# Performance work log

Hardware: AMD Instinct MI355X
Metric: run time of the kernel (lower is better)

## Reference

```python
import jax, jax.numpy as jnp
import numpy as np

NL, D, H, DK, L, F, P, NC, PS = 2, 128, 8, 16, 197, 256, 8, 1000, 16
EPS = 1e-5


def _ln(x, w, b):
    m = jnp.mean(x, -1, keepdims=True)
    v = jnp.mean((x - m) ** 2, -1, keepdims=True)
    return (x - m) * jax.lax.rsqrt(v + EPS) * w + b


def _trop_lin(x, W, b):
    # max-plus (tropical) linear: y_o = max_i (x_i + W[o, i]) + b_o
    return jnp.max(x[..., None, :] + W, axis=-1) + b


def _forward(x, patch_w, patch_b, cls_token, pos_embed, bn_gamma, bn_beta, bn_run_max, bn_run_range,
             n1_w, n1_b, n2_w, n2_b, wq, bq, wk, bk, wv, bv, wo, bo, gate_w, gate_b, temp,
             tu_w, tu_b, lf_a, lf_c, lf_gate, cu_w, cu_b, fg_w, fg_b, dn_w, dn_b,
             fn_w, fn_b, head_w, head_b):
    B, C, Hh, Ww = x.shape
    p = PS
    # patchify: [B,C,H,W] -> [B,num_patches,C*p*p]
    xp = x.reshape(B, C, Hh // p, p, Ww // p, p).transpose(0, 2, 4, 1, 3, 5).reshape(B, -1, C * p * p)
    h = xp @ patch_w.T + patch_b
    h = jnp.concatenate([jnp.broadcast_to(cls_token, (B, 1, D)), h], axis=1) + pos_embed
    # TropicalBatchNorm (eval mode, running buffers)
    h = bn_gamma * ((h - bn_run_max) / (bn_run_range + EPS)) + bn_beta
    scale = DK ** -0.5
    for i in range(NL):
        hn = _ln(h, n1_w[i], n1_b[i])
        Q = _trop_lin(hn, wq[i], bq[i]).reshape(B, L, H, DK).transpose(0, 2, 1, 3)
        K = _trop_lin(hn, wk[i], bk[i]).reshape(B, L, H, DK).transpose(0, 2, 1, 3)
        V = (hn @ wv[i].T + bv[i]).reshape(B, L, H, DK).transpose(0, 2, 1, 3)
        cs = jnp.einsum('bhqd,bhkd->bhqk', Q, K) * scale
        # tropical max-plus scores: max_d(Q_q + K_k)  -> [B,H,L,L]
        ts = jnp.max(Q[:, :, :, None, :] + K[:, :, None, :, :], axis=-1) * scale
        g = jax.nn.sigmoid(hn @ gate_w[i].T + gate_b[i]).transpose(0, 2, 1)[..., None]  # [B,H,L,1]
        attn = jax.nn.softmax((g * ts + (1.0 - g) * cs) / temp[i][None, :, None, None], axis=-1)
        out = jnp.einsum('bhqk,bhkd->bhqd', attn, V).transpose(0, 2, 1, 3).reshape(B, L, D)
        h = h + (out @ wo[i].T + bo[i])
        hn2 = _ln(h, n2_w[i], n2_b[i])
        z = _trop_lin(hn2, tu_w[i], tu_b[i])                 # [B,L,F]
        zp = z[:, :, None, :] * lf_a[i] + lf_c[i]            # [B,L,P,F]
        gl = jax.nn.sigmoid(lf_gate[i])
        trop = gl * jnp.max(zp, axis=2) + (1.0 - gl) * jnp.min(zp, axis=2)
        classical = jax.nn.gelu(hn2 @ cu_w[i].T + cu_b[i], approximate=False)
        gf = jax.nn.sigmoid(hn2 @ fg_w[i].T + fg_b[i])
        fused = gf * trop + (1.0 - gf) * classical
        h = h + (fused @ dn_w[i].T + dn_b[i])
    h = _ln(h, fn_w, fn_b)
    return h[:, 0] @ head_w.T + head_b


def setup_inputs() -> dict:
    ks = iter(jax.random.split(jax.random.key(0), 64))
    rn = lambda shape, s=0.02: jax.random.normal(next(ks), shape, jnp.float32) * s
    return dict(
        x=jax.random.normal(next(ks), (4, 3, 224, 224), jnp.float32),
        patch_w=rn((D, 3 * PS * PS)), patch_b=jnp.zeros((D,), jnp.float32),
        cls_token=rn((1, 1, D)), pos_embed=rn((1, L, D)),
        bn_gamma=jnp.ones((D,), jnp.float32), bn_beta=jnp.zeros((D,), jnp.float32),
        bn_run_max=jnp.zeros((D,), jnp.float32), bn_run_range=jnp.ones((D,), jnp.float32),
        n1_w=jnp.ones((NL, D), jnp.float32) + rn((NL, D)), n1_b=rn((NL, D)),
        n2_w=jnp.ones((NL, D), jnp.float32) + rn((NL, D)), n2_b=rn((NL, D)),
        wq=rn((NL, D, D)), bq=rn((NL, D)),
        wk=rn((NL, D, D)), bk=rn((NL, D)),
        wv=rn((NL, D, D)), bv=rn((NL, D)),
        wo=rn((NL, D, D)), bo=rn((NL, D)),
        gate_w=rn((NL, H, D)), gate_b=2.0 + rn((NL, H)),
        temp=1.0 + 0.1 * jax.random.uniform(next(ks), (NL, H), jnp.float32),
        tu_w=rn((NL, F, D)), tu_b=rn((NL, F)),
        lf_a=rn((NL, P, F), 0.5), lf_c=rn((NL, P, F), 0.1), lf_gate=rn((NL, F), 0.5),
        cu_w=rn((NL, F, D)), cu_b=rn((NL, F)),
        fg_w=rn((NL, F, D)), fg_b=2.0 + rn((NL, F)),
        dn_w=rn((NL, D, F)), dn_b=rn((NL, D)),
        fn_w=jnp.ones((D,), jnp.float32) + rn((D,)), fn_b=rn((D,)),
        head_w=rn((NC, D)), head_b=jnp.zeros((NC,), jnp.float32),
    )


def reference(x, patch_w, patch_b, cls_token, pos_embed, bn_gamma, bn_beta, bn_run_max, bn_run_range,
              n1_w, n1_b, n2_w, n2_b, wq, bq, wk, bk, wv, bv, wo, bo, gate_w, gate_b, temp,
              tu_w, tu_b, lf_a, lf_c, lf_gate, cu_w, cu_b, fg_w, fg_b, dn_w, dn_b,
              fn_w, fn_b, head_w, head_b):
    return _forward(x, patch_w, patch_b, cls_token, pos_embed, bn_gamma, bn_beta, bn_run_max, bn_run_range,
                    n1_w, n1_b, n2_w, n2_b, wq, bq, wk, bk, wv, bv, wo, bo, gate_w, gate_b, temp,
                    tu_w, tu_b, lf_a, lf_c, lf_gate, cu_w, cu_b, fg_w, fg_b, dn_w, dn_b,
                    fn_w, fn_b, head_w, head_b)
```

## Files before the change

### kernel.cpp

```cpp
#include <hip/hip_runtime.h>
#include <math.h>

#define EPSF 1e-5f

__device__ __forceinline__ float sigm(float v){ return 1.f/(1.f+__expf(-v)); }

#define WS_H    0
#define WS_Q    100864
#define WS_K    201728
#define WS_V    302592
#define WS_G    403456
#define WS_AO   409760
#define WS_PWT  510624
#define WS_WQT  608928
#define WS_WKT  641696
#define WS_WVT  674464
#define WS_WOT  707232
#define WS_GWT  740000
#define WS_TUT  742048
#define WS_CUT  807584
#define WS_FGT  873120
#define WS_DNT  938656
#define WS_HDT  1004192

__global__ __launch_bounds__(256) void k_tr(
    const float* __restrict__ pw, const float* __restrict__ wq, const float* __restrict__ wk,
    const float* __restrict__ wv, const float* __restrict__ wo, const float* __restrict__ gw,
    const float* __restrict__ tu, const float* __restrict__ cu, const float* __restrict__ fg,
    const float* __restrict__ dn, const float* __restrict__ hd, float* __restrict__ ws)
{
    __shared__ float tile[32][33];
    int tn = blockIdx.x, t = threadIdx.x;

    if (tn >= 608) {
        for (int i=t;i<2048;i+=256){
            int m=i>>10, rem=i&1023, k=rem>>3, hh=rem&7;
            ws[WS_GWT + m*1024 + k*8 + hh] = gw[m*1024 + hh*128 + k];
        }
        return;
    }

    const float* srcp; long dstoff; int N, K, NR, nt, kt;
    if (tn < 96) {
        srcp=pw; dstoff=WS_PWT; N=128; K=768; NR=128; nt=tn/24; kt=tn%24;
    } else if (tn < 224) {
        int i2=tn-96, inst=i2>>4, lt=i2&15, m2=inst>>1;
        srcp = (m2==0)?wq:(m2==1)?wk:(m2==2)?wv:wo;
        srcp += (inst&1)*16384;
        dstoff = WS_WQT + (long)m2*32768 + (inst&1)*16384;
        N=128; K=128; NR=128; nt=lt>>2; kt=lt&3;
    } else if (tn < 416) {
        int i2=tn-224, inst=i2>>5, lt=i2&31, m2=inst>>1;
        srcp = (m2==0)?tu:(m2==1)?cu:fg;
        srcp += (inst&1)*32768;
        dstoff = WS_TUT + (long)m2*65536 + (inst&1)*32768;
        N=256; K=128; NR=256; nt=lt>>2; kt=lt&3;
    } else if (tn < 480) {
        int i2=tn-416, inst=i2>>5, lt=i2&31;
        srcp = dn + inst*32768; dstoff = WS_DNT + (long)inst*32768;
        N=128; K=256; NR=128; nt=lt>>3; kt=lt&7;
    } else {
        int lt=tn-480; srcp=hd; dstoff=WS_HDT; N=1000; K=128; NR=1000; nt=lt>>2; kt=lt&3;
    }

    int n0=nt*32, k0=kt*32;
    int tr=t>>3, tc=(t&7)*4;
    float4 v={0.f,0.f,0.f,0.f};
    if (n0+tr < NR) v = *(const float4*)(srcp + (size_t)(n0+tr)*K + k0 + tc);
    tile[tr][tc]=v.x; tile[tr][tc+1]=v.y; tile[tr][tc+2]=v.z; tile[tr][tc+3]=v.w;
    __syncthreads();
    int kr=t>>3, nc=(t&7)*4;
    float o0=tile[nc][kr], o1=tile[nc+1][kr], o2=tile[nc+2][kr], o3=tile[nc+3][kr];
    float* dp = ws + dstoff + (size_t)(k0+kr)*N + n0 + nc;
    if (n0+nc+3 < NR) {
        float4 o4={o0,o1,o2,o3};
        *(float4*)dp = o4;
    } else {
        if (n0+nc   < NR) dp[0]=o0;
        if (n0+nc+1 < NR) dp[1]=o1;
        if (n0+nc+2 < NR) dp[2]=o2;
        if (n0+nc+3 < NR) dp[3]=o3;
    }
}

__device__ __forceinline__ void ln_rows(const float hv[4],
    const float* __restrict__ lw, const float* __restrict__ lb,
    float* hnS, float* red, int t)
{
    int d = t & 127;
    if (t < 128) {
        float s[4], s2[4];
        #pragma unroll
        for (int r=0;r<4;++r){ s[r]=hv[r]; s2[r]=hv[r]*hv[r]; }
        #pragma unroll
        for (int o=1;o<64;o<<=1){
            #pragma unroll
            for (int r=0;r<4;++r){ s[r]+=__shfl_xor(s[r],o); s2[r]+=__shfl_xor(s2[r],o); }
        }
        if ((t & 63)==0){
            int wid = t>>6;
            #pragma unroll
            for (int r=0;r<4;++r){ red[r*2+wid]=s[r]; red[8+r*2+wid]=s2[r]; }
        }
    }
    __syncthreads();
    if (t < 128) {
        #pragma unroll
        for (int r=0;r<4;++r){
            float S=red[r*2]+red[r*2+1], S2=red[8+r*2]+red[8+r*2+1];
            float mu=S*(1.f/128.f), var=S2*(1.f/128.f)-mu*mu;
            float rr=rsqrtf(var+EPSF);
            hnS[r*128+d]=(hv[r]-mu)*rr*lw[d]+lb[d];
        }
    }
    __syncthreads();
}

__device__ __forceinline__ void qkvT512(const float* hnS, float* pacc, int r0, int t,
    const float* __restrict__ wqT, const float* __restrict__ bq,
    const float* __restrict__ wkT, const float* __restrict__ bk,
    const float* __restrict__ wvT, const float* __restrict__ bv,
    const float* __restrict__ gwT, const float* __restrict__ gb,
    float* __restrict__ Q, float* __restrict__ Kg, float* __restrict__ V,
    float* __restrict__ g)
{
    if (t < 384) {
        int mat = t >> 7, q4i = t & 31, ks = (t >> 5) & 3;
        const float* wT = (mat==0) ? wqT : (mat==1) ? wkT : wvT;
        const float4* w4 = (const float4*)wT + q4i;
        float4 acc[4];
        if (mat < 2) {
            #pragma unroll
            for (int r=0;r<4;++r){ acc[r].x=acc[r].y=acc[r].z=acc[r].w=-1e30f; }
            #pragma unroll
            for (int kb=0;kb<4;++kb){
                float4 wv8[8];
                #pragma unroll
                for (int j=0;j<8;++j) wv8[j]=w4[(ks*32+kb*8+j)*32];
                #pragma unroll
                for (int j=0;j<8;++j){
                    float4 w=wv8[j];
                    #pragma unroll
                    for (int r=0;r<4;++r){
                        float av = hnS[r*128 + ks*32+kb*8+j];
                        acc[r].x=fmaxf(acc[r].x,av+w.x); acc[r].y=fmaxf(acc[r].y,av+w.y);
                        acc[r].z=fmaxf(acc[r].z,av+w.z); acc[r].w=fmaxf(acc[r].w,av+w.w);
                    }
                }
            }
        } else {
            #pragma unroll
            for (int r=0;r<4;++r){ acc[r].x=acc[r].y=acc[r].z=acc[r].w=0.f; }
            #pragma unroll
            for (int kb=0;kb<4;++kb){
                float4 wv8[8];
                #pragma unroll
                for (int j=0;j<8;++j) wv8[j]=w4[(ks*32+kb*8+j)*32];
                #pragma unroll
                for (int j=0;j<8;++j){
                    float4 w=wv8[j];
                    #pragma unroll
                    for (int r=0;r<4;++r){
                        float av = hnS[r*128 + ks*32+kb*8+j];
                        acc[r].x=fmaf(av,w.x,acc[r].x); acc[r].y=fmaf(av,w.y,acc[r].y);
                        acc[r].z=fmaf(av,w.z,acc[r].z); acc[r].w=fmaf(av,w.w,acc[r].w);
                    }
                }
            }
        }
        #pragma unroll
        for (int r=0;r<4;++r)
            *(float4*)(pacc + mat*2048 + ks*512 + r*128 + q4i*4) = acc[r];
    } else {
        int u = t & 127, r = u>>5, hh=(u>>2)&7, ks=u&3;
        const float* a = hnS + r*128;
        float acc = 0.f;
        #pragma unroll
        for (int kb=0;kb<4;++kb){
            float wv8[8];
            #pragma unroll
            for (int j=0;j<8;++j) wv8[j]=gwT[(ks*32+kb*8+j)*8+hh];
            #pragma unroll
            for (int j=0;j<8;++j) acc = fmaf(a[ks*32+kb*8+j], wv8[j], acc);
        }
        acc += __shfl_xor(acc,1);
        acc += __shfl_xor(acc,2);
        if (ks==0) g[(r0+r)*8+hh] = sigm(acc + gb[hh]);
    }
    __syncthreads();
    if (t < 384) {
        int mat=t>>7, d=t&127;
        float* dst = (mat==0) ? Q : (mat==1) ? Kg : V;
        const float* bias = (mat==0) ? bq : (mat==1) ? bk : bv;
        #pragma unroll
        for (int r=0;r<4;++r){
            float p0 = pacc[mat*2048 + 0*512 + r*128 + d];
            float p1 = pacc[mat*2048 + 1*512 + r*128 + d];
            float p2 = pacc[mat*2048 + 2*512 + r*128 + d];
            float p3 = pacc[mat*2048 + 3*512 + r*128 + d];
            float s = (mat < 2) ? fmaxf(fmaxf(p0,p1), fmaxf(p2,p3))
                                : (p0 + p1 + p2 + p3);
            dst[(size_t)(r0+r)*128 + d] = s + bias[d];
        }
    }
}

__global__ __launch_bounds__(512) void k_p1(
    const float* __restrict__ x, const float* __restrict__ pwT, const float* __restrict__ pb,
    const float* __restrict__ clsT, const float* __restrict__ pos,
    const float* __restrict__ bng, const float* __restrict__ bnb,
    const float* __restrict__ bnm, const float* __restrict__ bnr,
    const float* __restrict__ n1w, const float* __restrict__ n1b,
    const float* __restrict__ wqT, const float* __restrict__ bq,
    const float* __restrict__ wkT, const float* __restrict__ bk,
    const float* __restrict__ wvT, const float* __restrict__ bv,
    const float* __restrict__ gwT, const float* __restrict__ gb,
    float* __restrict__ h, float* __restrict__ Q, float* __restrict__ Kg,
    float* __restrict__ V, float* __restrict__ g)
{
    __shared__ __align__(16) float xp[4*768];
    __shared__ __align__(16) float pacc[8192];
    __shared__ __align__(16) float hnS[512];
    __shared__ float red[16];
    int t = threadIdx.x, r0 = blockIdx.x * 4;

    #pragma unroll
    for (int r=0;r<4;++r){
        int row=r0+r, b=row/197, l=row-b*197;
        if (l>0){
            int patch=l-1, ph=patch/14, pc=patch-ph*14;
            const float* xb = x + (size_t)b*150528 + ph*3584 + pc*16;
            for (int i=t;i<768;i+=512){
                int c=i>>8, rr=(i>>4)&15, cc=i&15;
                xp[r*768+i] = xb[c*50176 + rr*224 + cc];
            }
        }
    }
    __syncthreads();

    {
        int q4i = t & 31, ks = t >> 5;
        float4 acc[4];
        #pragma unroll
        for (int r=0;r<4;++r){ acc[r].x=acc[r].y=acc[r].z=acc[r].w=0.f; }
        const float4* w4 = (const float4*)pwT + q4i;
        #pragma unroll
        for (int kb=0;kb<6;++kb){
            float4 wv8[8];
            #pragma unroll
            for (int j=0;j<8;++j) wv8[j]=w4[(ks*48+kb*8+j)*32];
            #pragma unroll
            for (int j=0;j<8;++j){
                float4 w=wv8[j];
                #pragma unroll
                for (int r=0;r<4;++r){
                    float av = xp[r*768 + ks*48+kb*8+j];
                    acc[r].x=fmaf(av,w.x,acc[r].x); acc[r].y=fmaf(av,w.y,acc[r].y);
                    acc[r].z=fmaf(av,w.z,acc[r].z); acc[r].w=fmaf(av,w.w,acc[r].w);
                }
            }
        }
        #pragma unroll
        for (int r=0;r<4;++r)
            *(float4*)(pacc + (ks*4+r)*128 + q4i*4) = acc[r];
    }
    __syncthreads();

    float hres[4]={0.f,0.f,0.f,0.f};
    if (t < 128){
        int d=t;
        #pragma unroll
        for (int r=0;r<4;++r){
            int row=r0+r, l=row%197;
            float s = 0.f;
            #pragma unroll
            for (int ks=0;ks<16;++ks) s += pacc[(ks*4+r)*128+d];
            float v = (l==0) ? clsT[d] : (s + pb[d]);
            v += pos[l*128+d];
            v = bng[d]*((v-bnm[d])/(bnr[d]+EPSF))+bnb[d];
            hres[r]=v;
            h[row*128+d]=v;
        }
    }
    ln_rows(hres, n1w, n1b, hnS, red, t);
    qkvT512(hnS, pacc, r0, t, wqT,bq,wkT,bk,wvT,bv,gwT,gb, Q,Kg,V,g);
}

__global__ __launch_bounds__(256) void k_attn(
    const float* __restrict__ Qd, const float* __restrict__ Kd,
    const float* __restrict__ Vd, const float* __restrict__ gd,
    const float* __restrict__ tempL, float* __restrict__ ao)
{
    __shared__ __align__(16) float Ks[197*20];
    __shared__ __align__(16) float Vs[197*20];
    int bid = blockIdx.x, t = threadIdx.x;
    int qc = bid % 7, bh = bid / 7, hh = bh & 7, b = bh >> 3;
    size_t base = (size_t)(b*197)*128 + hh*16;

    {
        const float4* ksrc=(const float4*)(Kd+base);
        const float4* vsrc=(const float4*)(Vd+base);
        float4* kdst=(float4*)Ks; float4* vdst=(float4*)Vs;
        for (int idx=t; idx<788; idx+=256){
            int l=idx>>2, jj=idx&3;
            kdst[l*5+jj]=ksrc[l*32+jj];
            vdst[l*5+jj]=vsrc[l*32+jj];
        }
    }
    __syncthreads();

    int q = qc*32 + (t>>3), j8 = t&7;
    if (q >= 197) return;

    float Qr[16];
    {
        const float4* qp=(const float4*)(Qd+base+(size_t)q*128);
        #pragma unroll
        for (int u=0;u<4;++u){
            float4 v=qp[u];
            Qr[4*u]=v.x; Qr[4*u+1]=v.y; Qr[4*u+2]=v.z; Qr[4*u+3]=v.w;
        }
    }
    float gq = gd[(b*197+q)*8+hh];
    float it = 0.25f / tempL[hh];
    float gg = gq*it, cg = (1.f-gq)*it;

    float m=-1e30f, lsum=0.f, o[16];
    #pragma unroll
    for (int j=0;j<16;++j) o[j]=0.f;

    for (int k=j8;k<197;k+=8){
        const float4* kr4=(const float4*)(Ks+k*20);
        float4 kv0=kr4[0], kv1=kr4[1], kv2=kr4[2], kv3=kr4[3];
        float kr[16] = {kv0.x,kv0.y,kv0.z,kv0.w, kv1.x,kv1.y,kv1.z,kv1.w,
                        kv2.x,kv2.y,kv2.z,kv2.w, kv3.x,kv3.y,kv3.z,kv3.w};
        float cs=0.f, ts=-1e30f;
        #pragma unroll
        for (int j=0;j<16;++j){
            cs=fmaf(Qr[j],kr[j],cs);
            ts=fmaxf(ts,Qr[j]+kr[j]);
        }
        float sc=fmaf(gg,ts,cg*cs);
        if (sc>m){
            float c=__expf(m-sc);
            lsum*=c;
            #pragma unroll
            for (int j=0;j<16;++j) o[j]*=c;
            m=sc;
        }
        float p=__expf(sc-m);
        lsum+=p;
        const float4* vr4=(const float4*)(Vs+k*20);
        float4 vv0=vr4[0], vv1=vr4[1], vv2=vr4[2], vv3=vr4[3];
        float vr[16] = {vv0.x,vv0.y,vv0.z,vv0.w, vv1.x,vv1.y,vv1.z,vv1.w,
                        vv2.x,vv2.y,vv2.z,vv2.w, vv3.x,vv3.y,vv3.z,vv3.w};
        #pragma unroll
        for (int j=0;j<16;++j) o[j]=fmaf(p,vr[j],o[j]);
    }

    #pragma unroll
    for (int mask=1;mask<8;mask<<=1){
        float mo=__shfl_xor(m,mask), lo=__shfl_xor(lsum,mask);
        float mn=fmaxf(m,mo);
        float ea=__expf(m-mn), eb=__expf(mo-mn);
        lsum=lsum*ea+lo*eb;
        #pragma unroll
        for (int j=0;j<16;++j){
            float oo=__shfl_xor(o[j],mask);
            o[j]=o[j]*ea+oo*eb;
        }
        m=mn;
    }

    if (j8==0){
        float inv=1.f/lsum;
        float* orow=ao+base+(size_t)q*128;
        #pragma unroll
        for (int j=0;j<16;++j) orow[j]=o[j]*inv;
    }
}

template <int FINAL>
__global__ __launch_bounds__(512) void k_p34(
    const float* __restrict__ ao, float* __restrict__ h,
    const float* __restrict__ woT, const float* __restrict__ bo,
    const float* __restrict__ n2w, const float* __restrict__ n2b,
    const float* __restrict__ tuT, const float* __restrict__ tub,
    const float* __restrict__ laA, const float* __restrict__ laC,
    const float* __restrict__ lgG,
    const float* __restrict__ cuT, const float* __restrict__ cub,
    const float* __restrict__ fgT, const float* __restrict__ fgb,
    const float* __restrict__ dnT, const float* __restrict__ dnb,
    const float* __restrict__ nlw, const float* __restrict__ nlb,
    const float* __restrict__ wqT, const float* __restrict__ bq,
    const float* __restrict__ wkT, const float* __restrict__ bk,
    const float* __restrict__ wvT, const float* __restrict__ bv,
    const float* __restrict__ gwT, const float* __restrict__ gb,
    float* __restrict__ Q, float* __restrict__ Kg, float* __restrict__ V,
    float* __restrict__ g,
    const float* __restrict__ hdT, const float* __restrict__ hdb,
    float* __restrict__ out)
{
    __shared__ __align__(16) float aoS[512];
    __shared__ __align__(16) float pacc[8192];
    __shared__ __align__(16) float hnS[512];
    __shared__ __align__(16) float zP[6144];
    __shared__ __align__(16) float fusedS[1024];
    __shared__ float red[16];
    int t = threadIdx.x, r0 = blockIdx.x * 4;

    aoS[t] = ao[(size_t)r0*128 + t];
    __syncthreads();

    {
        int q4i=t&31, ks=t>>5;
        float4 acc[4];
        #pragma unroll
        for (int r=0;r<4;++r){ acc[r].x=acc[r].y=acc[r].z=acc[r].w=0.f; }
        const float4* w4=(const float4*)woT + q4i;
        float4 wv8[8];
        #pragma unroll
        for (int j=0;j<8;++j) wv8[j]=w4[(ks*8+j)*32];
        #pragma unroll
        for (int j=0;j<8;++j){
            float4 w=wv8[j];
            #pragma unroll
            for (int r=0;r<4;++r){
                float av=aoS[r*128 + ks*8+j];
                acc[r].x=fmaf(av,w.x,acc[r].x); acc[r].y=fmaf(av,w.y,acc[r].y);
                acc[r].z=fmaf(av,w.z,acc[r].z); acc[r].w=fmaf(av,w.w,acc[r].w);
            }
        }
        #pragma unroll
        for (int r=0;r<4;++r)
            *(float4*)(pacc + (ks*4+r)*128 + q4i*4) = acc[r];
    }
    __syncthreads();

    float hres[4]={0.f,0.f,0.f,0.f};
    if (t<128){
        int d=t;
        #pragma unroll
        for (int r=0;r<4;++r){
            float s=0.f;
            #pragma unroll
            for (int ks=0;ks<16;++ks) s += pacc[(ks*4+r)*128+d];
            hres[r]=h[(r0+r)*128+d]+s+bo[d];
        }
    }
    ln_rows(hres, n2w, n2b, hnS, red, t);

    {
        int gidx=t>>6, fq=t&63;
        if (gidx < 6) {
            int mat=gidx>>1, ks2=gidx&1;
            const float* wT = (mat==0)? tuT : (mat==1)? cuT : fgT;
            const float4* w4=(const float4*)wT + fq;
            float4 acc[4];
            if (mat==0){
                #pragma unroll
                for (int r=0;r<4;++r){ acc[r].x=acc[r].y=acc[r].z=acc[r].w=-1e30f; }
                #pragma unroll
                for (int kb=0;kb<8;++kb){
                    float4 wv8[8];
                    #pragma unroll
                    for (int j=0;j<8;++j) wv8[j]=w4[(ks2*64+kb*8+j)*64];
                    #pragma unroll
                    for (int j=0;j<8;++j){
                        float4 w=wv8[j];
                        #pragma unroll
                        for (int r=0;r<4;++r){
                            float av=hnS[r*128 + ks2*64+kb*8+j];
                            acc[r].x=fmaxf(acc[r].x,av+w.x); acc[r].y=fmaxf(acc[r].y,av+w.y);
                            acc[r].z=fmaxf(acc[r].z,av+w.z); acc[r].w=fmaxf(acc[r].w,av+w.w);
                        }
                    }
                }
            } else {
                #pragma unroll
                for (int r=0;r<4;++r){ acc[r].x=acc[r].y=acc[r].z=acc[r].w=0.f; }
                #pragma unroll
                for (int kb=0;kb<8;++kb){
                    float4 wv8[8];
                    #pragma unroll
                    for (int j=0;j<8;++j) wv8[j]=w4[(ks2*64+kb*8+j)*64];
                    #pragma unroll
                    for (int j=0;j<8;++j){
                        float4 w=wv8[j];
                        #pragma unroll
                        for (int r=0;r<4;++r){
                            float av=hnS[r*128 + ks2*64+kb*8+j];
                            acc[r].x=fmaf(av,w.x,acc[r].x); acc[r].y=fmaf(av,w.y,acc[r].y);
                            acc[r].z=fmaf(av,w.z,acc[r].z); acc[r].w=fmaf(av,w.w,acc[r].w);
                        }
                    }
                }
            }
            #pragma unroll
            for (int r=0;r<4;++r)
                *(float4*)(zP + mat*2048 + ks2*1024 + r*256 + fq*4) = acc[r];
        }
    }
    __syncthreads();

    #pragma unroll
    for (int s2=0;s2<2;++s2){
        int slot = t + s2*512;
        int r = slot>>8, f = slot&255;
        float z  = fmaxf(zP[r*256+f],        zP[1024+r*256+f]) + tub[f];
        float xc = zP[2048+r*256+f] + zP[3072+r*256+f] + cub[f];
        float gv = zP[4096+r*256+f] + zP[5120+r*256+f] + fgb[f];
        float gl = sigm(lgG[f]);
        float mx=-1e30f, mn=1e30f;
        #pragma unroll
        for (int p=0;p<8;++p){
            float zp=fmaf(z, laA[p*256+f], laC[p*256+f]);
            mx=fmaxf(mx,zp); mn=fminf(mn,zp);
        }
        float trop=gl*mx+(1.f-gl)*mn;
        float cla=0.5f*xc*(1.f+erff(xc*0.70710678118654752f));
        float gf=sigm(gv);
        fusedS[r*256+f]=gf*trop+(1.f-gf)*cla;
    }
    __syncthreads();

    {
        int q4i=t&31, ks=t>>5;
        float4 acc[4];
        #pragma unroll
        for (int r=0;r<4;++r){ acc[r].x=acc[r].y=acc[r].z=acc[r].w=0.f; }
        const float4* w4=(const float4*)dnT + q4i;
        #pragma unroll
        for (int kb=0;kb<2;++kb){
            float4 wv8[8];
            #pragma unroll
            for (int j=0;j<8;++j) wv8[j]=w4[(ks*16+kb*8+j)*32];
            #pragma unroll
            for (int j=0;j<8;++j){
                float4 w=wv8[j];
                #pragma unroll
                for (int r=0;r<4;++r){
                    float av=fusedS[r*256 + ks*16+kb*8+j];
                    acc[r].x=fmaf(av,w.x,acc[r].x); acc[r].y=fmaf(av,w.y,acc[r].y);
                    acc[r].z=fmaf(av,w.z,acc[r].z); acc[r].w=fmaf(av,w.w,acc[r].w);
                }
            }
        }
        __syncthreads();
        #pragma unroll
        for (int r=0;r<4;++r)
            *(float4*)(pacc + (ks*4+r)*128 + q4i*4) = acc[r];
    }
    __syncthreads();
    if (t<128){
        int d=t;
        #pragma unroll
        for (int r=0;r<4;++r){
            float s=0.f;
            #pragma unroll
            for (int ks=0;ks<16;++ks) s += pacc[(ks*4+r)*128+d];
            hres[r]+=s+dnb[d];
            if (!FINAL) h[(r0+r)*128+d]=hres[r];
        }
    }
    ln_rows(hres, nlw, nlb, hnS, red, t);

    if (!FINAL) {
        qkvT512(hnS, pacc, r0, t, wqT,bq,wkT,bk,wvT,bv,gwT,gb, Q,Kg,V,g);
    } else {
        int crow=-1, cb2=0;
        #pragma unroll
        for (int r=0;r<4;++r){
            int row=r0+r;
            if (row==0 || row==197 || row==394 || row==591){ crow=r; cb2=row/197; }
        }
        if (crow>=0 && t<500){
            const float2* w2=(const float2*)hdT + t;
            const float* a = hnS + crow*128;
            float acc0=hdb[2*t], acc1=hdb[2*t+1];
            #pragma unroll
            for (int kb=0;kb<16;++kb){
                float2 wv8[8];
                #pragma unroll
                for (int j=0;j<8;++j) wv8[j]=w2[(kb*8+j)*500];
                #pragma unroll
                for (int j=0;j<8;++j){
                    float av=a[kb*8+j];
                    acc0=fmaf(av,wv8[j].x,acc0); acc1=fmaf(av,wv8[j].y,acc1);
                }
            }
            out[cb2*1000+2*t]=acc0;
            out[cb2*1000+2*t+1]=acc1;
        }
    }
}

extern "C" void kernel_launch(void* const* d_in, const int* in_sizes, int n_in,
                              void* d_out, int out_size, void* d_ws, size_t ws_size,
                              hipStream_t stream)
{
    const float* x        = (const float*)d_in[0];
    const float* patch_w  = (const float*)d_in[1];
    const float* patch_b  = (const float*)d_in[2];
    const float* cls_tok  = (const float*)d_in[3];
    const float* pos_emb  = (const float*)d_in[4];
    const float* bn_gamma = (const float*)d_in[5];
    const float* bn_beta  = (const float*)d_in[6];
    const float* bn_rmax  = (const float*)d_in[7];
    const float* bn_rrng  = (const float*)d_in[8];
    const float* n1_w     = (const float*)d_in[9];
    const float* n1_b     = (const float*)d_in[10];
    const float* n2_w     = (const float*)d_in[11];
    const float* n2_b     = (const float*)d_in[12];
    const float* wq       = (const float*)d_in[13];
    const float* bq       = (const float*)d_in[14];
    const float* wk       = (const float*)d_in[15];
    const float* bk       = (const float*)d_in[16];
    const float* wv       = (const float*)d_in[17];
    const float* bv       = (const float*)d_in[18];
    const float* wo       = (const float*)d_in[19];
    const float* bo       = (const float*)d_in[20];
    const float* gate_w   = (const float*)d_in[21];
    const float* gate_b   = (const float*)d_in[22];
    const float* temp     = (const float*)d_in[23];
    const float* tu_w     = (const float*)d_in[24];
    const float* tu_b     = (const float*)d_in[25];
    const float* lf_a     = (const float*)d_in[26];
    const float* lf_c     = (const float*)d_in[27];
    const float* lf_gate  = (const float*)d_in[28];
    const float* cu_w     = (const float*)d_in[29];
    const float* cu_b     = (const float*)d_in[30];
    const float* fg_w     = (const float*)d_in[31];
    const float* fg_b     = (const float*)d_in[32];
    const float* dn_w     = (const float*)d_in[33];
    const float* dn_b     = (const float*)d_in[34];
    const float* fn_w     = (const float*)d_in[35];
    const float* fn_b     = (const float*)d_in[36];
    const float* head_w   = (const float*)d_in[37];
    const float* head_b   = (const float*)d_in[38];

    float* ws = (float*)d_ws;
    float* h   = ws + WS_H;
    float* Q   = ws + WS_Q;
    float* Kb  = ws + WS_K;
    float* V   = ws + WS_V;
    float* g   = ws + WS_G;
    float* ao  = ws + WS_AO;
    float* out = (float*)d_out;

    k_tr<<<609, 256, 0, stream>>>(patch_w, wq, wk, wv, wo, gate_w,
                                  tu_w, cu_w, fg_w, dn_w, head_w, ws);

    k_p1<<<197, 512, 0, stream>>>(x, ws+WS_PWT, patch_b, cls_tok, pos_emb,
                                  bn_gamma, bn_beta, bn_rmax, bn_rrng,
                                  n1_w, n1_b,
                                  ws+WS_WQT, bq, ws+WS_WKT, bk, ws+WS_WVT, bv,
                                  ws+WS_GWT, gate_b,
                                  h, Q, Kb, V, g);

    k_attn<<<224, 256, 0, stream>>>(Q, Kb, V, g, temp, ao);

    k_p34<0><<<197, 512, 0, stream>>>(ao, h,
        ws+WS_WOT, bo, n2_w, n2_b,
        ws+WS_TUT, tu_b, lf_a, lf_c, lf_gate,
        ws+WS_CUT, cu_b, ws+WS_FGT, fg_b, ws+WS_DNT, dn_b,
        n1_w + 128, n1_b + 128,
        ws+WS_WQT+16384, bq + 128, ws+WS_WKT+16384, bk + 128,
        ws+WS_WVT+16384, bv + 128, ws+WS_GWT+1024, gate_b + 8,
        Q, Kb, V, g, nullptr, nullptr, nullptr);

    k_attn<<<224, 256, 0, stream>>>(Q, Kb, V, g, temp + 8, ao);

    k_p34<1><<<197, 512, 0, stream>>>(ao, h,
        ws+WS_WOT+16384, bo + 128, n2_w + 128, n2_b + 128,
        ws+WS_TUT+32768, tu_b + 256, lf_a + 2048, lf_c + 2048, lf_gate + 256,
        ws+WS_CUT+32768, cu_b + 256, ws+WS_FGT+32768, fg_b + 256,
        ws+WS_DNT+32768, dn_b + 128,
        fn_w, fn_b,
        nullptr, nullptr, nullptr, nullptr, nullptr, nullptr, nullptr, nullptr,
        Q, Kb, V, g, ws+WS_HDT, head_b, out);
}
```

Before: 79.33 us.

## Process eight token rows per block in row-wise kernels to improve weight reuse

The patch-embed/QKV kernel and the attention-output/FFN kernels now handle 8 rows per block instead of 4, halving the grid to 99 blocks. Each weight load from global memory is reused across twice as many rows, and all 512 threads now take part in the reductions and LayerNorm instead of only 128. Shared buffers are merged into one union array and boundary guards are added for the padded last block. In exchange, each thread holds more accumulator registers and the smaller grid leaves more compute units idle.

```diff
diff --git a/kernel.cpp b/kernel.cpp
--- a/kernel.cpp
+++ b/kernel.cpp
@@ -83,40 +83,33 @@
     }
 }
 
-__device__ __forceinline__ void ln_rows(const float hv[4],
+__device__ __forceinline__ void ln8(const float hv[2],
     const float* __restrict__ lw, const float* __restrict__ lb,
-    float* hnS, float* red, int t)
+    float* hnS, float* redS, float* redS2, int t)
 {
-    int d = t & 127;
-    if (t < 128) {
-        float s[4], s2[4];
-        #pragma unroll
-        for (int r=0;r<4;++r){ s[r]=hv[r]; s2[r]=hv[r]*hv[r]; }
-        #pragma unroll
-        for (int o=1;o<64;o<<=1){
-            #pragma unroll
-            for (int r=0;r<4;++r){ s[r]+=__shfl_xor(s[r],o); s2[r]+=__shfl_xor(s2[r],o); }
-        }
-        if ((t & 63)==0){
-            int wid = t>>6;
-            #pragma unroll
-            for (int r=0;r<4;++r){ red[r*2+wid]=s[r]; red[8+r*2+wid]=s2[r]; }
-        }
-    }
-    __syncthreads();
-    if (t < 128) {
-        #pragma unroll
-        for (int r=0;r<4;++r){
-            float S=red[r*2]+red[r*2+1], S2=red[8+r*2]+red[8+r*2+1];
-            float mu=S*(1.f/128.f), var=S2*(1.f/128.f)-mu*mu;
-            float rr=rsqrtf(var+EPSF);
-            hnS[r*128+d]=(hv[r]-mu)*rr*lw[d]+lb[d];
-        }
+    #pragma unroll
+    for (int s=0;s<2;++s){
+        float sm=hv[s], sq=hv[s]*hv[s];
+        #pragma unroll
+        for (int o=1;o<64;o<<=1){ sm+=__shfl_xor(sm,o); sq+=__shfl_xor(sq,o); }
+        if ((t&63)==0){
+            int slot=t+s*512, r=slot>>7, half=(t>>6)&1;
+            redS[r*2+half]=sm; redS2[r*2+half]=sq;
+        }
+    }
+    __syncthreads();
+    #pragma unroll
+    for (int s=0;s<2;++s){
+        int slot=t+s*512, r=slot>>7, d=slot&127;
+        float S=redS[r*2]+redS[r*2+1], S2=redS2[r*2]+redS2[r*2+1];
+        float mu=S*(1.f/128.f), var=S2*(1.f/128.f)-mu*mu;
+        float rr=rsqrtf(var+EPSF);
+        hnS[r*128+d]=(hv[s]-mu)*rr*lw[d]+lb[d];
     }
     __syncthreads();
 }
 
-__device__ __forceinline__ void qkvT512(const float* hnS, float* pacc, int r0, int t,
+__device__ __forceinline__ void qkvT8(const float* hnS, float* uni, int r0, int t,
     const float* __restrict__ wqT, const float* __restrict__ bq,
     const float* __restrict__ wkT, const float* __restrict__ bk,
     const float* __restrict__ wvT, const float* __restrict__ bv,
@@ -128,10 +121,10 @@
         int mat = t >> 7, q4i = t & 31, ks = (t >> 5) & 3;
         const float* wT = (mat==0) ? wqT : (mat==1) ? wkT : wvT;
         const float4* w4 = (const float4*)wT + q4i;
-        float4 acc[4];
+        float4 acc[8];
         if (mat < 2) {
             #pragma unroll
-            for (int r=0;r<4;++r){ acc[r].x=acc[r].y=acc[r].z=acc[r].w=-1e30f; }
+            for (int r=0;r<8;++r){ acc[r].x=acc[r].y=acc[r].z=acc[r].w=-1e30f; }
             #pragma unroll
             for (int kb=0;kb<4;++kb){
                 float4 wv8[8];
@@ -141,7 +134,7 @@
                 for (int j=0;j<8;++j){
                     float4 w=wv8[j];
                     #pragma unroll
-                    for (int r=0;r<4;++r){
+                    for (int r=0;r<8;++r){
                         float av = hnS[r*128 + ks*32+kb*8+j];
                         acc[r].x=fmaxf(acc[r].x,av+w.x); acc[r].y=fmaxf(acc[r].y,av+w.y);
                         acc[r].z=fmaxf(acc[r].z,av+w.z); acc[r].w=fmaxf(acc[r].w,av+w.w);
@@ -150,7 +143,7 @@
             }
         } else {
             #pragma unroll
-            for (int r=0;r<4;++r){ acc[r].x=acc[r].y=acc[r].z=acc[r].w=0.f; }
+            for (int r=0;r<8;++r){ acc[r].x=acc[r].y=acc[r].z=acc[r].w=0.f; }
             #pragma unroll
             for (int kb=0;kb<4;++kb){
                 float4 wv8[8];
@@ -160,7 +153,7 @@
                 for (int j=0;j<8;++j){
                     float4 w=wv8[j];
                     #pragma unroll
-                    for (int r=0;r<4;++r){
+                    for (int r=0;r<8;++r){
                         float av = hnS[r*128 + ks*32+kb*8+j];
                         acc[r].x=fmaf(av,w.x,acc[r].x); acc[r].y=fmaf(av,w.y,acc[r].y);
                         acc[r].z=fmaf(av,w.z,acc[r].z); acc[r].w=fmaf(av,w.w,acc[r].w);
@@ -169,23 +162,23 @@
             }
         }
         #pragma unroll
-        for (int r=0;r<4;++r)
-            *(float4*)(pacc + mat*2048 + ks*512 + r*128 + q4i*4) = acc[r];
+        for (int r=0;r<8;++r)
+            *(float4*)(uni + mat*4096 + ks*1024 + r*128 + q4i*4) = acc[r];
     } else {
-        int u = t & 127, r = u>>5, hh=(u>>2)&7, ks=u&3;
-        const float* a = hnS + r*128;
+        int u = t & 127, r8 = u>>4, hh=(u>>1)&7, ks2=u&1;
+        const float* a = hnS + r8*128;
         float acc = 0.f;
         #pragma unroll
-        for (int kb=0;kb<4;++kb){
+        for (int kb=0;kb<8;++kb){
             float wv8[8];
             #pragma unroll
-            for (int j=0;j<8;++j) wv8[j]=gwT[(ks*32+kb*8+j)*8+hh];
-            #pragma unroll
-            for (int j=0;j<8;++j) acc = fmaf(a[ks*32+kb*8+j], wv8[j], acc);
+            for (int j=0;j<8;++j) wv8[j]=gwT[(ks2*64+kb*8+j)*8+hh];
+            #pragma unroll
+            for (int j=0;j<8;++j) acc = fmaf(a[ks2*64+kb*8+j], wv8[j], acc);
         }
         acc += __shfl_xor(acc,1);
-        acc += __shfl_xor(acc,2);
-        if (ks==0) g[(r0+r)*8+hh] = sigm(acc + gb[hh]);
+        int row=r0+r8;
+        if (ks2==0 && row<788) g[row*8+hh] = sigm(acc + gb[hh]);
     }
     __syncthreads();
     if (t < 384) {
@@ -193,14 +186,15 @@
         float* dst = (mat==0) ? Q : (mat==1) ? Kg : V;
         const float* bias = (mat==0) ? bq : (mat==1) ? bk : bv;
         #pragma unroll
-        for (int r=0;r<4;++r){
-            float p0 = pacc[mat*2048 + 0*512 + r*128 + d];
-            float p1 = pacc[mat*2048 + 1*512 + r*128 + d];
-            float p2 = pacc[mat*2048 + 2*512 + r*128 + d];
-            float p3 = pacc[mat*2048 + 3*512 + r*128 + d];
+        for (int r=0;r<8;++r){
+            float p0 = uni[mat*4096 + 0*1024 + r*128 + d];
+            float p1 = uni[mat*4096 + 1*1024 + r*128 + d];
+            float p2 = uni[mat*4096 + 2*1024 + r*128 + d];
+            float p3 = uni[mat*4096 + 3*1024 + r*128 + d];
             float s = (mat < 2) ? fmaxf(fmaxf(p0,p1), fmaxf(p2,p3))
                                 : (p0 + p1 + p2 + p3);
-            dst[(size_t)(r0+r)*128 + d] = s + bias[d];
+            int row=r0+r;
+            if (row<788) dst[(size_t)row*128 + d] = s + bias[d];
         }
     }
 }
@@ -218,21 +212,24 @@
     float* __restrict__ h, float* __restrict__ Q, float* __restrict__ Kg,
     float* __restrict__ V, float* __restrict__ g)
 {
-    __shared__ __align__(16) float xp[4*768];
-    __shared__ __align__(16) float pacc[8192];
-    __shared__ __align__(16) float hnS[512];
-    __shared__ float red[16];
-    int t = threadIdx.x, r0 = blockIdx.x * 4;
-
-    #pragma unroll
-    for (int r=0;r<4;++r){
-        int row=r0+r, b=row/197, l=row-b*197;
-        if (l>0){
-            int patch=l-1, ph=patch/14, pc=patch-ph*14;
-            const float* xb = x + (size_t)b*150528 + ph*3584 + pc*16;
-            for (int i=t;i<768;i+=512){
-                int c=i>>8, rr=(i>>4)&15, cc=i&15;
-                xp[r*768+i] = xb[c*50176 + rr*224 + cc];
+    __shared__ __align__(16) float xp[8*768];
+    __shared__ __align__(16) float uni[16384];
+    __shared__ __align__(16) float hnS[1024];
+    __shared__ float redS[16], redS2[16];
+    int t = threadIdx.x, r0 = blockIdx.x * 8;
+
+    #pragma unroll
+    for (int r=0;r<8;++r){
+        int row=r0+r;
+        if (row < 788){
+            int b=row/197, l=row-b*197;
+            if (l>0){
+                int patch=l-1, ph=patch/14, pc=patch-ph*14;
+                const float* xb = x + (size_t)b*150528 + ph*3584 + pc*16;
+                for (int i=t;i<768;i+=512){
+                    int c=i>>8, rr=(i>>4)&15, cc=i&15;
+                    xp[r*768+i] = xb[c*50176 + rr*224 + cc];
+                }
             }
         }
     }
@@ -240,9 +237,9 @@
 
     {
         int q4i = t & 31, ks = t >> 5;
-        float4 acc[4];
-        #pragma unroll
-        for (int r=0;r<4;++r){ acc[r].x=acc[r].y=acc[r].z=acc[r].w=0.f; }
+        float4 acc[8];
+        #pragma unroll
+        for (int r=0;r<8;++r){ acc[r].x=acc[r].y=acc[r].z=acc[r].w=0.f; }
         const float4* w4 = (const float4*)pwT + q4i;
         #pragma unroll
         for (int kb=0;kb<6;++kb){
@@ -253,7 +250,7 @@
             for (int j=0;j<8;++j){
                 float4 w=wv8[j];
                 #pragma unroll
-                for (int r=0;r<4;++r){
+                for (int r=0;r<8;++r){
                     float av = xp[r*768 + ks*48+kb*8+j];
                     acc[r].x=fmaf(av,w.x,acc[r].x); acc[r].y=fmaf(av,w.y,acc[r].y);
                     acc[r].z=fmaf(av,w.z,acc[r].z); acc[r].w=fmaf(av,w.w,acc[r].w);
@@ -261,29 +258,28 @@
             }
         }
         #pragma unroll
-        for (int r=0;r<4;++r)
-            *(float4*)(pacc + (ks*4+r)*128 + q4i*4) = acc[r];
-    }
-    __syncthreads();
-
-    float hres[4]={0.f,0.f,0.f,0.f};
-    if (t < 128){
-        int d=t;
-        #pragma unroll
-        for (int r=0;r<4;++r){
-            int row=r0+r, l=row%197;
-            float s = 0.f;
-            #pragma unroll
-            for (int ks=0;ks<16;++ks) s += pacc[(ks*4+r)*128+d];
-            float v = (l==0) ? clsT[d] : (s + pb[d]);
-            v += pos[l*128+d];
-            v = bng[d]*((v-bnm[d])/(bnr[d]+EPSF))+bnb[d];
-            hres[r]=v;
-            h[row*128+d]=v;
-        }
-    }
-    ln_rows(hres, n1w, n1b, hnS, red, t);
-    qkvT512(hnS, pacc, r0, t, wqT,bq,wkT,bk,wvT,bv,gwT,gb, Q,Kg,V,g);
+        for (int r=0;r<8;++r)
+            *(float4*)(uni + (ks*8+r)*128 + q4i*4) = acc[r];
+    }
+    __syncthreads();
+
+    float hres[2];
+    #pragma unroll
+    for (int s=0;s<2;++s){
+        int slot=t+s*512, r=slot>>7, d=slot&127;
+        int row=r0+r, l=row%197;
+        float sm = 0.f;
+        #pragma unroll
+        for (int ks=0;ks<16;++ks) sm += uni[(ks*8+r)*128+d];
+        float v = (l==0) ? clsT[d] : (sm + pb[d]);
+        v += pos[l*128+d];
+        v = bng[d]*((v-bnm[d])/(bnr[d]+EPSF))+bnb[d];
+        hres[s]=v;
+        if (row<788) h[(size_t)row*128+d]=v;
+    }
+    __syncthreads();
+    ln8(hres, n1w, n1b, hnS, redS, redS2, t);
+    qkvT8(hnS, uni, r0, t, wqT,bq,wkT,bk,wvT,bv,gwT,gb, Q,Kg,V,g);
 }
 
 __global__ __launch_bounds__(256) void k_attn(
@@ -401,22 +397,22 @@
     const float* __restrict__ hdT, const float* __restrict__ hdb,
     float* __restrict__ out)
 {
-    __shared__ __align__(16) float aoS[512];
-    __shared__ __align__(16) float pacc[8192];
-    __shared__ __align__(16) float hnS[512];
-    __shared__ __align__(16) float zP[6144];
-    __shared__ __align__(16) float fusedS[1024];
-    __shared__ float red[16];
-    int t = threadIdx.x, r0 = blockIdx.x * 4;
-
-    aoS[t] = ao[(size_t)r0*128 + t];
+    __shared__ __align__(16) float aoS[1024];
+    __shared__ __align__(16) float uni[16384];
+    __shared__ __align__(16) float hnS[1024];
+    __shared__ __align__(16) float fusedS[2048];
+    __shared__ float redS[16], redS2[16];
+    int t = threadIdx.x, r0 = blockIdx.x * 8;
+
+    aoS[t]     = ao[(size_t)r0*128 + t];
+    aoS[t+512] = ao[(size_t)r0*128 + t + 512];
     __syncthreads();
 
     {
         int q4i=t&31, ks=t>>5;
-        float4 acc[4];
-        #pragma unroll
-        for (int r=0;r<4;++r){ acc[r].x=acc[r].y=acc[r].z=acc[r].w=0.f; }
+        float4 acc[8];
+        #pragma unroll
+        for (int r=0;r<8;++r){ acc[r].x=acc[r].y=acc[r].z=acc[r].w=0.f; }
         const float4* w4=(const float4*)woT + q4i;
         float4 wv8[8];
         #pragma unroll
@@ -425,30 +421,29 @@
         for (int j=0;j<8;++j){
             float4 w=wv8[j];
             #pragma unroll
-            for (int r=0;r<4;++r){
+            for (int r=0;r<8;++r){
                 float av=aoS[r*128 + ks*8+j];
                 acc[r].x=fmaf(av,w.x,acc[r].x); acc[r].y=fmaf(av,w.y,acc[r].y);
                 acc[r].z=fmaf(av,w.z,acc[r].z); acc[r].w=fmaf(av,w.w,acc[r].w);
             }
         }
         #pragma unroll
-        for (int r=0;r<4;++r)
-            *(float4*)(pacc + (ks*4+r)*128 + q4i*4) = acc[r];
-    }
-    __syncthreads();
-
-    float hres[4]={0.f,0.f,0.f,0.f};
-    if (t<128){
-        int d=t;
-        #pragma unroll
-        for (int r=0;r<4;++r){
-            float s=0.f;
-            #pragma unroll
-            for (int ks=0;ks<16;++ks) s += pacc[(ks*4+r)*128+d];
-            hres[r]=h[(r0+r)*128+d]+s+bo[d];
-        }
-    }
-    ln_rows(hres, n2w, n2b, hnS, red, t);
+        for (int r=0;r<8;++r)
+            *(float4*)(uni + (ks*8+r)*128 + q4i*4) = acc[r];
+    }
+    __syncthreads();
+
+    float hres[2];
+    #pragma unroll
+    for (int s=0;s<2;++s){
+        int slot=t+s*512, r=slot>>7, d=slot&127;
+        float sm=0.f;
+        #pragma unroll
+        for (int ks=0;ks<16;++ks) sm += uni[(ks*8+r)*128+d];
+        hres[s] = h[(size_t)(r0+r)*128+d] + sm + bo[d];
+    }
+    __syncthreads();
+    ln8(hres, n2w, n2b, hnS, redS, redS2, t);
 
     {
         int gidx=t>>6, fq=t&63;
@@ -456,10 +451,10 @@
             int mat=gidx>>1, ks2=gidx&1;
             const float* wT = (mat==0)? tuT : (mat==1)? cuT : fgT;
             const float4* w4=(const float4*)wT + fq;
-            float4 acc[4];
+            float4 acc[8];
             if (mat==0){
                 #pragma unroll
-                for (int r=0;r<4;++r){ acc[r].x=acc[r].y=acc[r].z=acc[r].w=-1e30f; }
+                for (int r=0;r<8;++r){ acc[r].x=acc[r].y=acc[r].z=acc[r].w=-1e30f; }
                 #pragma unroll
                 for (int kb=0;kb<8;++kb){
                     float4 wv8[8];
@@ -469,7 +464,7 @@
                     for (int j=0;j<8;++j){
                         float4 w=wv8[j];
                         #pragma unroll
-                        for (int r=0;r<4;++r){
+                        for (int r=0;r<8;++r){
                             float av=hnS[r*128 + ks2*64+kb*8+j];
                             acc[r].x=fmaxf(acc[r].x,av+w.x); acc[r].y=fmaxf(acc[r].y,av+w.y);
                             acc[r].z=fmaxf(acc[r].z,av+w.z); acc[r].w=fmaxf(acc[r].w,av+w.w);
@@ -478,7 +473,7 @@
                 }
             } else {
                 #pragma unroll
-                for (int r=0;r<4;++r){ acc[r].x=acc[r].y=acc[r].z=acc[r].w=0.f; }
+                for (int r=0;r<8;++r){ acc[r].x=acc[r].y=acc[r].z=acc[r].w=0.f; }
                 #pragma unroll
                 for (int kb=0;kb<8;++kb){
                     float4 wv8[8];
@@ -488,7 +483,7 @@
                     for (int j=0;j<8;++j){
                         float4 w=wv8[j];
                         #pragma unroll
-                        for (int r=0;r<4;++r){
+                        for (int r=0;r<8;++r){
                             float av=hnS[r*128 + ks2*64+kb*8+j];
                             acc[r].x=fmaf(av,w.x,acc[r].x); acc[r].y=fmaf(av,w.y,acc[r].y);
                             acc[r].z=fmaf(av,w.z,acc[r].z); acc[r].w=fmaf(av,w.w,acc[r].w);
@@ -497,19 +492,19 @@
                 }
             }
             #pragma unroll
-            for (int r=0;r<4;++r)
-                *(float4*)(zP + mat*2048 + ks2*1024 + r*256 + fq*4) = acc[r];
-        }
-    }
-    __syncthreads();
-
-    #pragma unroll
-    for (int s2=0;s2<2;++s2){
+            for (int r=0;r<8;++r)
+                *(float4*)(uni + mat*4096 + ks2*2048 + r*256 + fq*4) = acc[r];
+        }
+    }
+    __syncthreads();
+
+    #pragma unroll
+    for (int s2=0;s2<4;++s2){
         int slot = t + s2*512;
         int r = slot>>8, f = slot&255;
-        float z  = fmaxf(zP[r*256+f],        zP[1024+r*256+f]) + tub[f];
-        float xc = zP[2048+r*256+f] + zP[3072+r*256+f] + cub[f];
-        float gv = zP[4096+r*256+f] + zP[5120+r*256+f] + fgb[f];
+        float z  = fmaxf(uni[r*256+f],          uni[2048+r*256+f]) + tub[f];
+        float xc = uni[4096+r*256+f]  + uni[4096+2048+r*256+f]  + cub[f];
+        float gv = uni[8192+r*256+f]  + uni[8192+2048+r*256+f]  + fgb[f];
         float gl = sigm(lgG[f]);
         float mx=-1e30f, mn=1e30f;
         #pragma unroll
@@ -526,9 +521,9 @@
 
     {
         int q4i=t&31, ks=t>>5;
-        float4 acc[4];
-        #pragma unroll
-        for (int r=0;r<4;++r){ acc[r].x=acc[r].y=acc[r].z=acc[r].w=0.f; }
+        float4 acc[8];
+        #pragma unroll
+        for (int r=0;r<8;++r){ acc[r].x=acc[r].y=acc[r].z=acc[r].w=0.f; }
         const float4* w4=(const float4*)dnT + q4i;
         #pragma unroll
         for (int kb=0;kb<2;++kb){
@@ -539,7 +534,7 @@
             for (int j=0;j<8;++j){
                 float4 w=wv8[j];
                 #pragma unroll
-                for (int r=0;r<4;++r){
+                for (int r=0;r<8;++r){
                     float av=fusedS[r*256 + ks*16+kb*8+j];
                     acc[r].x=fmaf(av,w.x,acc[r].x); acc[r].y=fmaf(av,w.y,acc[r].y);
                     acc[r].z=fmaf(av,w.z,acc[r].z); acc[r].w=fmaf(av,w.w,acc[r].w);
@@ -548,31 +543,31 @@
         }
         __syncthreads();
         #pragma unroll
-        for (int r=0;r<4;++r)
-            *(float4*)(pacc + (ks*4+r)*128 + q4i*4) = acc[r];
-    }
-    __syncthreads();
-    if (t<128){
-        int d=t;
-        #pragma unroll
-        for (int r=0;r<4;++r){
-            float s=0.f;
-            #pragma unroll
-            for (int ks=0;ks<16;++ks) s += pacc[(ks*4+r)*128+d];
-            hres[r]+=s+dnb[d];
-            if (!FINAL) h[(r0+r)*128+d]=hres[r];
-        }
-    }
-    ln_rows(hres, nlw, nlb, hnS, red, t);
+        for (int r=0;r<8;++r)
+            *(float4*)(uni + (ks*8+r)*128 + q4i*4) = acc[r];
+    }
+    __syncthreads();
+    #pragma unroll
+    for (int s=0;s<2;++s){
+        int slot=t+s*512, r=slot>>7, d=slot&127;
+        float sm=0.f;
+        #pragma unroll
+        for (int ks=0;ks<16;++ks) sm += uni[(ks*8+r)*128+d];
+        hres[s] += sm + dnb[d];
+        int row=r0+r;
+        if (!FINAL && row<788) h[(size_t)row*128+d]=hres[s];
+    }
+    __syncthreads();
+    ln8(hres, nlw, nlb, hnS, redS, redS2, t);
 
     if (!FINAL) {
-        qkvT512(hnS, pacc, r0, t, wqT,bq,wkT,bk,wvT,bv,gwT,gb, Q,Kg,V,g);
+        qkvT8(hnS, uni, r0, t, wqT,bq,wkT,bk,wvT,bv,gwT,gb, Q,Kg,V,g);
     } else {
         int crow=-1, cb2=0;
         #pragma unroll
-        for (int r=0;r<4;++r){
+        for (int r=0;r<8;++r){
             int row=r0+r;
-            if (row==0 || row==197 || row==394 || row==591){ crow=r; cb2=row/197; }
+            if (row<788 && row%197==0){ crow=r; cb2=row/197; }
         }
         if (crow>=0 && t<500){
             const float2* w2=(const float2*)hdT + t;
@@ -651,16 +646,16 @@
     k_tr<<<609, 256, 0, stream>>>(patch_w, wq, wk, wv, wo, gate_w,
                                   tu_w, cu_w, fg_w, dn_w, head_w, ws);
 
-    k_p1<<<197, 512, 0, stream>>>(x, ws+WS_PWT, patch_b, cls_tok, pos_emb,
-                                  bn_gamma, bn_beta, bn_rmax, bn_rrng,
-                                  n1_w, n1_b,
-                                  ws+WS_WQT, bq, ws+WS_WKT, bk, ws+WS_WVT, bv,
-                                  ws+WS_GWT, gate_b,
-                                  h, Q, Kb, V, g);
+    k_p1<<<99, 512, 0, stream>>>(x, ws+WS_PWT, patch_b, cls_tok, pos_emb,
+                                 bn_gamma, bn_beta, bn_rmax, bn_rrng,
+                                 n1_w, n1_b,
+                                 ws+WS_WQT, bq, ws+WS_WKT, bk, ws+WS_WVT, bv,
+                                 ws+WS_GWT, gate_b,
+                                 h, Q, Kb, V, g);
 
     k_attn<<<224, 256, 0, stream>>>(Q, Kb, V, g, temp, ao);
 
-    k_p34<0><<<197, 512, 0, stream>>>(ao, h,
+    k_p34<0><<<99, 512, 0, stream>>>(ao, h,
         ws+WS_WOT, bo, n2_w, n2_b,
         ws+WS_TUT, tu_b, lf_a, lf_c, lf_gate,
         ws+WS_CUT, cu_b, ws+WS_FGT, fg_b, ws+WS_DNT, dn_b,
@@ -671,7 +666,7 @@
 
     k_attn<<<224, 256, 0, stream>>>(Q, Kb, V, g, temp + 8, ao);
 
-    k_p34<1><<<197, 512, 0, stream>>>(ao, h,
+    k_p34<1><<<99, 512, 0, stream>>>(ao, h,
         ws+WS_WOT+16384, bo + 128, n2_w + 128, n2_b + 128,
         ws+WS_TUT+32768, tu_b + 256, lf_a + 2048, lf_c + 2048, lf_gate + 256,
         ws+WS_CUT+32768, cu_b + 256, ws+WS_FGT+32768, fg_b + 256,
```

Measured after the change: 98.60 us. 24.3% more time.
